# Kernel optimization log

Measured on AMD Instinct MI355X. Metric: run time of the kernel, lower is better.

## Reference

```python
import jax, jax.numpy as jnp
import numpy as np

C = 64
K = 3  # kernel_size
B, H, W = 8, 128, 128


def conv2d(x, w, b, pad, groups=1):
    y = jax.lax.conv_general_dilated(
        x, w, window_strides=(1, 1), padding=[(pad, pad), (pad, pad)],
        feature_group_count=groups, dimension_numbers=('NCHW', 'OIHW', 'NCHW'))
    return y + b[None, :, None, None]


def setup_inputs() -> dict:
    key = jax.random.key(0)
    ks = jax.random.split(key, 11)
    s3 = 1.0 / np.sqrt(C * 9)  # kaiming-ish scale for 3x3 convs
    inp = {
        'x':  jax.random.normal(ks[0], (B, C, H, W), jnp.float32),
        'w0': jax.random.normal(ks[1], (C, C, 3, 3), jnp.float32) * s3,
        'b0': jax.random.normal(ks[2], (C,), jnp.float32) * 0.01,
        'w1': jax.random.normal(ks[3], (C, 1, 3, 3), jnp.float32) * (1.0 / 3.0),  # depthwise
        'b1': jax.random.normal(ks[4], (C,), jnp.float32) * 0.01,
        'w2': jax.random.normal(ks[5], (1, 1, K), jnp.float32) * (1.0 / np.sqrt(K)),  # conv1d over channel axis
        'b2': jax.random.normal(ks[6], (1,), jnp.float32) * 0.01,
        'w3': jax.random.normal(ks[7], (C * K * K, C, 1, 1), jnp.float32) * (1.0 / np.sqrt(C)),  # 1x1 -> dynamic filters
        'b3': jax.random.normal(ks[8], (C * K * K,), jnp.float32) * 0.01,
        'wf': jax.random.normal(ks[9], (C, C, 3, 3), jnp.float32) * s3,
        'bf': jax.random.normal(ks[10], (C,), jnp.float32) * 0.01,
    }
    return inp


def reference(x, w0, b0, w1, b1, w2, b2, w3, b3, wf, bf):
    b, c, h, w = x.shape
    pre = x
    # conv0: dense 3x3
    x0 = conv2d(x, w0, b0, pad=1)
    # conv1: depthwise 3x3
    x1 = conv2d(x0, w1, b1, pad=1, groups=c)
    # ECA-style channel attention: global avg pool -> conv1d over channel dim
    m = jnp.mean(x0, axis=(2, 3))  # [b, c]
    x2 = jax.lax.conv_general_dilated(
        m[:, None, :], w2, window_strides=(1,), padding=[(K // 2, K // 2)],
        dimension_numbers=('NCH', 'OIH', 'NCH')) + b2[None, :, None]  # [b, 1, c]
    out = x1 + x2[:, 0, :, None, None]  # broadcast [b,c,1,1] over h,w
    # conv3: 1x1 producing per-pixel dynamic filters [b, c*9, h, w]
    fil = jnp.einsum('oc,bchw->bohw', w3[:, :, 0, 0], out) + b3[None, :, None, None]
    filter_x = fil.reshape(b, c, K * K, h, w)
    # unfold(x0): 3x3 patches, channel-major then row-major kernel positions
    xp = jnp.pad(x0, ((0, 0), (0, 0), (1, 1), (1, 1)))
    unfold_x = jnp.stack(
        [xp[:, :, i:i + h, j:j + w] for i in range(3) for j in range(3)], axis=2)  # [b,c,9,h,w]
    out = jnp.sum(unfold_x * filter_x, axis=2)  # per-pixel dynamic conv
    out = jnp.where(out >= 0, out, 0.2 * out)  # LeakyReLU(0.2)
    out = conv2d(out, wf, bf, pad=1) + pre
    return out
```

## Files before the change

kernel.cpp:

```cpp
#include <hip/hip_runtime.h>

#define BB 8
#define C 64
#define HH 128
#define WW 128
#define HW (HH*WW)

#define TS 72
#define NPX 324
#define FNPX 340

typedef __attribute__((ext_vector_type(8))) short short8;
typedef __attribute__((ext_vector_type(4))) short short4v;
typedef __attribute__((ext_vector_type(4))) float f32x4;

__device__ inline unsigned short f2bf(float f) {
    union { float f; unsigned u; } v; v.f = f;
    unsigned r = v.u + 0x7fff + ((v.u >> 16) & 1);
    return (unsigned short)(r >> 16);
}
__device__ inline float bf2f(unsigned short h) {
    union { unsigned u; float f; } v; v.u = ((unsigned)h) << 16;
    return v.f;
}

__global__ __launch_bounds__(256) void prep_kernel(
    const float* __restrict__ w0, const float* __restrict__ wf,
    const float* __restrict__ w3, const float* __restrict__ b3,
    unsigned short* __restrict__ wb0, unsigned short* __restrict__ wbf,
    unsigned short* __restrict__ wb3, float* __restrict__ b3r,
    float* __restrict__ m)
{
    const int t = blockIdx.x * 256 + threadIdx.x;
    for (int i = t; i < C*C*9; i += 32*256) {
        int p = i % 9; int rest = i / 9; int ci = rest % C; int oc = rest / C;
        wb0[(p*C + oc)*C + ci] = f2bf(w0[i]);
        wbf[(p*C + oc)*C + ci] = f2bf(wf[i]);
    }
    for (int i = t; i < 9*C*C; i += 32*256) {
        int j = i >> 12, oc = (i >> 6) & 63, k = i & 63;
        wb3[i] = f2bf(w3[(oc*9 + j)*C + k]);
    }
    for (int i = t; i < 9*C; i += 32*256) {
        int j = i >> 6, oc = i & 63;
        b3r[i] = b3[oc*9 + j];
    }
    for (int i = t; i < BB*C; i += 32*256) m[i] = 0.f;
}

__global__ __launch_bounds__(256) void nhwc_kernel(
    const float* __restrict__ x, unsigned short* __restrict__ xb)
{
    const int px = blockIdx.x * 256 + threadIdx.x;
    const int b = px >> 14, pin = px & 16383;
    const float* sp = x + (size_t)b*C*HW + pin;
    unsigned short* dp = xb + (size_t)px*C;
#pragma unroll
    for (int g = 0; g < 8; ++g) {
        short8 o;
#pragma unroll
        for (int k = 0; k < 8; ++k) o[k] = (short)f2bf(sp[(size_t)(g*8+k)*HW]);
        *(short8*)&dp[g*8] = o;
    }
}

__global__ __launch_bounds__(512) void conv0_kernel(
    const unsigned short* __restrict__ xb,
    const unsigned short* __restrict__ wb,
    const float* __restrict__ bias,
    unsigned short* __restrict__ x0g,
    float* __restrict__ msum)
{
    __shared__ unsigned short tile[NPX*TS];
    __shared__ float red[8][64];
    const int b  = blockIdx.z;
    const int h0 = blockIdx.y * 16;
    const int w0 = blockIdx.x * 16;
    const int t  = threadIdx.x;

    {
        const int pxi = t & 63, g = t >> 6;
        for (int px = pxi; px < NPX; px += 64) {
            int th = px / 18, tw = px - th*18;
            int gh = h0 + th - 1, gw = w0 + tw - 1;
            short8 v = {0,0,0,0,0,0,0,0};
            if ((unsigned)gh < HH && (unsigned)gw < WW)
                v = *(const short8*)&xb[((size_t)(b*HW) + gh*WW + gw)*C + g*8];
            *(short8*)&tile[px*TS + g*8] = v;
        }
    }
    __syncthreads();

    const int wid = t >> 6, ln = t & 63;
    const int l15 = ln & 15, q = ln >> 4;

    f32x4 acc[2][4];
#pragma unroll
    for (int nt = 0; nt < 2; ++nt)
#pragma unroll
        for (int mt = 0; mt < 4; ++mt) acc[nt][mt] = (f32x4){0.f,0.f,0.f,0.f};

#pragma unroll
    for (int p = 0; p < 9; ++p) {
        const int dh = p / 3, dw = p % 3;
#pragma unroll
        for (int ks = 0; ks < 2; ++ks) {
            short8 af[4];
#pragma unroll
            for (int mt = 0; mt < 4; ++mt)
                af[mt] = *(const short8*)&wb[((size_t)(p*C) + mt*16 + l15)*C + ks*32 + q*8];
            short8 bf[2];
#pragma unroll
            for (int nt = 0; nt < 2; ++nt)
                bf[nt] = *(const short8*)&tile[((wid*2+nt+dh)*18 + l15 + dw)*TS + ks*32 + q*8];
#pragma unroll
            for (int nt = 0; nt < 2; ++nt)
#pragma unroll
                for (int mt = 0; mt < 4; ++mt)
                    acc[nt][mt] = __builtin_amdgcn_mfma_f32_16x16x32_bf16(
                        af[mt], bf[nt], acc[nt][mt], 0, 0, 0);
        }
    }

#pragma unroll
    for (int nt = 0; nt < 2; ++nt) {
        const int hh = h0 + wid*2 + nt;
        const size_t base = ((size_t)(b*HW) + hh*WW + w0 + l15)*C;
#pragma unroll
        for (int mt = 0; mt < 4; ++mt) {
            const int oc0 = mt*16 + q*4;
            const float4 bv = *(const float4*)&bias[oc0];
            unsigned u0 = (unsigned)f2bf(acc[nt][mt][0] + bv.x)
                        | ((unsigned)f2bf(acc[nt][mt][1] + bv.y) << 16);
            unsigned u1 = (unsigned)f2bf(acc[nt][mt][2] + bv.z)
                        | ((unsigned)f2bf(acc[nt][mt][3] + bv.w) << 16);
            uint2 uu; uu.x = u0; uu.y = u1;
            *(uint2*)&x0g[base + oc0] = uu;
        }
    }

    f32x4 s[4];
#pragma unroll
    for (int mt = 0; mt < 4; ++mt)
#pragma unroll
        for (int reg = 0; reg < 4; ++reg)
            s[mt][reg] = acc[0][mt][reg] + acc[1][mt][reg];
#pragma unroll
    for (int mask = 1; mask < 16; mask <<= 1)
#pragma unroll
        for (int mt = 0; mt < 4; ++mt)
#pragma unroll
            for (int reg = 0; reg < 4; ++reg)
                s[mt][reg] += __shfl_xor(s[mt][reg], mask);
    if (l15 == 0) {
#pragma unroll
        for (int mt = 0; mt < 4; ++mt)
#pragma unroll
            for (int reg = 0; reg < 4; ++reg)
                red[wid][mt*16 + q*4 + reg] = s[mt][reg];
    }
    __syncthreads();
    if (t < 64) {
        float tot = bias[t] * 256.f;
#pragma unroll
        for (int w = 0; w < 8; ++w) tot += red[w][t];
        atomicAdd(&msum[b*C + t], tot);
    }
}

__global__ __launch_bounds__(512) void fused_dyn_kernel(
    const unsigned short* __restrict__ x0,
    const float* __restrict__ w1, const float* __restrict__ b1,
    const float* __restrict__ w2, const float* __restrict__ b2,
    const unsigned short* __restrict__ wb3,
    const float* __restrict__ b3r,
    const float* __restrict__ m,
    unsigned short* __restrict__ yg)
{
    __shared__ unsigned short tile[NPX*TS];
    __shared__ unsigned short alds[256*64];
    const int b  = blockIdx.z;
    const int h0 = blockIdx.y * 16;
    const int w0 = blockIdx.x * 16;
    const int t  = threadIdx.x;

    {
        const int pxi = t & 63, g = t >> 6;
        for (int px = pxi; px < NPX; px += 64) {
            int th = px / 18, tw = px - th*18;
            int gh = h0 + th - 1, gw = w0 + tw - 1;
            short8 v = {0,0,0,0,0,0,0,0};
            if ((unsigned)gh < HH && (unsigned)gw < WW)
                v = *(const short8*)&x0[((size_t)(b*HW) + gh*WW + gw)*C + g*8];
            *(short8*)&tile[px*TS + g*8] = v;
        }
    }
    __syncthreads();

    {
        const int px = t & 255, ghalf = t >> 8;
        const int r = px >> 4, cc = px & 15;
        const unsigned short* tb = tile + (r*18 + cc)*TS;
        const float w2a = w2[0], w2b = w2[1], w2c = w2[2], b2v = b2[0];
        const float inv = 1.f / (float)HW;
        const int sw = px & 7;
#pragma unroll
        for (int g = 0; g < 4; ++g) {
            const int octet = ghalf*4 + g;
            float dw8[8];
#pragma unroll
            for (int k = 0; k < 8; ++k) dw8[k] = 0.f;
#pragma unroll
            for (int j = 0; j < 9; ++j) {
                short8 v = *(const short8*)&tb[((j/3)*18 + (j%3))*TS + octet*8];
#pragma unroll
                for (int k = 0; k < 8; ++k)
                    dw8[k] = fmaf(w1[(octet*8+k)*9 + j],
                                  bf2f((unsigned short)v[k]), dw8[k]);
            }
            short8 o;
#pragma unroll
            for (int k = 0; k < 8; ++k) {
                const int c = octet*8 + k;
                const float mc = m[b*C + c] * inv;
                const float mp = (c > 0)  ? m[b*C + c - 1] * inv : 0.f;
                const float mn = (c < 63) ? m[b*C + c + 1] * inv : 0.f;
                const float att = fmaf(w2a, mp, fmaf(w2b, mc, fmaf(w2c, mn, b2v)));
                o[k] = (short)f2bf(dw8[k] + b1[c] + att);
            }
            *(short8*)&alds[px*64 + ((octet ^ sw) * 8)] = o;
        }
    }
    __syncthreads();

    const int wid = t >> 6, ln = t & 63;
    const int l15 = ln & 15, q = ln >> 4;
    const int rl0 = (wid & 3) * 4;
    const int ogh = wid >> 2;

    short8 pfrag[4][2];
#pragma unroll
    for (int nt = 0; nt < 4; ++nt) {
        const int p = (rl0 + nt)*16 + l15;
        const int psw = p & 7;
#pragma unroll
        for (int ks = 0; ks < 2; ++ks)
            pfrag[nt][ks] = *(const short8*)&alds[p*64 + (((ks*4 + q) ^ psw) * 8)];
    }

#pragma unroll
    for (int ogi = 0; ogi < 2; ++ogi) {
        const int og = ogh*2 + ogi;
        f32x4 yac[4];
#pragma unroll
        for (int nt = 0; nt < 4; ++nt) yac[nt] = (f32x4){0.f,0.f,0.f,0.f};

        for (int j = 0; j < 9; ++j) {
            const int dh = j / 3, dw = j - dh*3;
            const f32x4 seed = *(const f32x4*)&b3r[j*64 + og*16 + q*4];
            const size_t abase = ((size_t)(j*64 + og*16 + l15))*C;
            const short8 a0 = *(const short8*)&wb3[abase + q*8];
            const short8 a1 = *(const short8*)&wb3[abase + 32 + q*8];
#pragma unroll
            for (int nt = 0; nt < 4; ++nt) {
                f32x4 fil = __builtin_amdgcn_mfma_f32_16x16x32_bf16(
                    a0, pfrag[nt][0], seed, 0, 0, 0);
                fil = __builtin_amdgcn_mfma_f32_16x16x32_bf16(
                    a1, pfrag[nt][1], fil, 0, 0, 0);
                const short4v pv = *(const short4v*)
                    &tile[((rl0+nt+dh)*18 + l15 + dw)*TS + og*16 + q*4];
#pragma unroll
                for (int reg = 0; reg < 4; ++reg)
                    yac[nt][reg] = fmaf(fil[reg],
                        bf2f((unsigned short)pv[reg]), yac[nt][reg]);
            }
        }

#pragma unroll
        for (int nt = 0; nt < 4; ++nt) {
            const size_t base = ((size_t)(b*HW) + (h0+rl0+nt)*WW + w0 + l15)*C;
            f32x4 v = yac[nt];
#pragma unroll
            for (int reg = 0; reg < 4; ++reg)
                v[reg] = (v[reg] >= 0.f) ? v[reg] : 0.2f * v[reg];
            unsigned u0 = (unsigned)f2bf(v[0]) | ((unsigned)f2bf(v[1]) << 16);
            unsigned u1 = (unsigned)f2bf(v[2]) | ((unsigned)f2bf(v[3]) << 16);
            uint2 uu; uu.x = u0; uu.y = u1;
            *(uint2*)&yg[base + og*16 + q*4] = uu;
        }
    }
}

__global__ __launch_bounds__(512) void convf_kernel(
    const unsigned short* __restrict__ yg,
    const unsigned short* __restrict__ wb,
    const float* __restrict__ bias,
    const float* __restrict__ res,
    float* __restrict__ outg)
{
    __shared__ unsigned short tile[FNPX*TS];
    const int b  = blockIdx.z;
    const int h0 = blockIdx.y * 8;
    const int w0 = blockIdx.x * 32;
    const int t  = threadIdx.x;

    {
        const int pxi = t & 63, g = t >> 6;
        for (int px = pxi; px < FNPX; px += 64) {
            int th = px / 34, tw = px - th*34;
            int gh = h0 + th - 1, gw = w0 + tw - 1;
            short8 v = {0,0,0,0,0,0,0,0};
            if ((unsigned)gh < HH && (unsigned)gw < WW)
                v = *(const short8*)&yg[((size_t)(b*HW) + gh*WW + gw)*C + g*8];
            *(short8*)&tile[px*TS + g*8] = v;
        }
    }
    __syncthreads();

    const int wid = t >> 6, ln = t & 63;
    const int l15 = ln & 15, q = ln >> 4;

    f32x4 acc[2][4];
#pragma unroll
    for (int mg = 0; mg < 2; ++mg)
#pragma unroll
        for (int nt = 0; nt < 4; ++nt) acc[mg][nt] = (f32x4){0.f,0.f,0.f,0.f};

#pragma unroll
    for (int p = 0; p < 9; ++p) {
        const int dh = p / 3, dw = p % 3;
#pragma unroll
        for (int ks = 0; ks < 2; ++ks) {
            short8 bfrag[4];
#pragma unroll
            for (int nt = 0; nt < 4; ++nt)
                bfrag[nt] = *(const short8*)&wb[((size_t)(p*C) + nt*16 + l15)*C + ks*32 + q*8];
            short8 afrag[2];
#pragma unroll
            for (int mg = 0; mg < 2; ++mg)
                afrag[mg] = *(const short8*)&tile[((wid+dh)*34 + mg*16 + l15 + dw)*TS + ks*32 + q*8];
#pragma unroll
            for (int mg = 0; mg < 2; ++mg)
#pragma unroll
                for (int nt = 0; nt < 4; ++nt)
                    acc[mg][nt] = __builtin_amdgcn_mfma_f32_16x16x32_bf16(
                        afrag[mg], bfrag[nt], acc[mg][nt], 0, 0, 0);
        }
    }

#pragma unroll
    for (int mg = 0; mg < 2; ++mg) {
#pragma unroll
        for (int nt = 0; nt < 4; ++nt) {
            const int oc = nt*16 + l15;
            const float bv = bias[oc];
            const size_t base = (size_t)(b*C + oc)*HW + (h0+wid)*WW + w0 + mg*16 + q*4;
            const float4 rv = *(const float4*)&res[base];
            float4 ov;
            ov.x = acc[mg][nt][0] + bv + rv.x;
            ov.y = acc[mg][nt][1] + bv + rv.y;
            ov.z = acc[mg][nt][2] + bv + rv.z;
            ov.w = acc[mg][nt][3] + bv + rv.w;
            *(float4*)&outg[base] = ov;
        }
    }
}

extern "C" void kernel_launch(void* const* d_in, const int* in_sizes, int n_in,
                              void* d_out, int out_size, void* d_ws, size_t ws_size,
                              hipStream_t stream) {
    const float* x  = (const float*)d_in[0];
    const float* w0 = (const float*)d_in[1];
    const float* b0 = (const float*)d_in[2];
    const float* w1 = (const float*)d_in[3];
    const float* b1 = (const float*)d_in[4];
    const float* w2 = (const float*)d_in[5];
    const float* b2 = (const float*)d_in[6];
    const float* w3 = (const float*)d_in[7];
    const float* b3 = (const float*)d_in[8];
    const float* wf = (const float*)d_in[9];
    const float* bf = (const float*)d_in[10];
    float* out = (float*)d_out;

    unsigned short* x0  = (unsigned short*)d_ws;
    unsigned short* y   = x0  + (size_t)BB*HW*C;
    unsigned short* xb  = y   + (size_t)BB*HW*C;
    float*          m   = (float*)(xb + (size_t)BB*HW*C);
    unsigned short* wb0 = (unsigned short*)(m + BB*C);
    unsigned short* wbf = wb0 + 9*C*C;
    unsigned short* wb3 = wbf + 9*C*C;
    float*          b3r = (float*)(wb3 + 9*C*C);

    prep_kernel<<<32, 256, 0, stream>>>(w0, wf, w3, b3, wb0, wbf, wb3, b3r, m);
    nhwc_kernel<<<512, 256, 0, stream>>>(x, xb);
    conv0_kernel<<<dim3(8,8,8), 512, 0, stream>>>(xb, wb0, b0, x0, m);
    fused_dyn_kernel<<<dim3(8,8,8), 512, 0, stream>>>(
        x0, w1, b1, w2, b2, wb3, b3r, m, y);
    convf_kernel<<<dim3(4,16,8), 512, 0, stream>>>(y, wbf, bf, x, out);
}
```

Measured before the change: 248.2 us.

## Halve spatial tiles and block size; batch all halo loads before LDS stores

Each of the three conv kernels now uses half-height tiles with 256 threads instead of 512, doubling the grid to 1024 blocks so more blocks fit per CU and the GPU fills better. The halo tile load is rewritten so every thread issues all of its global loads into registers before any LDS store, putting more memory requests in flight. The cost is a larger fraction of redundant halo rows per output, twice as many atomics into the channel-mean sum, and changed warp-to-work mapping in the dynamic-filter stage.

```diff
diff --git a/kernel.cpp b/kernel.cpp
--- a/kernel.cpp
+++ b/kernel.cpp
@@ -7,8 +7,8 @@
 #define HW (HH*WW)
 
 #define TS 72
-#define NPX 324
-#define FNPX 340
+#define NPXC 180
+#define NPXF 204
 
 typedef __attribute__((ext_vector_type(8))) short short8;
 typedef __attribute__((ext_vector_type(4))) short short4v;
@@ -64,29 +64,39 @@
     }
 }
 
-__global__ __launch_bounds__(512) void conv0_kernel(
+__global__ __launch_bounds__(256) void conv0_kernel(
     const unsigned short* __restrict__ xb,
     const unsigned short* __restrict__ wb,
     const float* __restrict__ bias,
     unsigned short* __restrict__ x0g,
     float* __restrict__ msum)
 {
-    __shared__ unsigned short tile[NPX*TS];
-    __shared__ float red[8][64];
+    __shared__ unsigned short tile[NPXC*TS];
+    __shared__ float red[4][64];
     const int b  = blockIdx.z;
-    const int h0 = blockIdx.y * 16;
+    const int h0 = blockIdx.y * 8;
     const int w0 = blockIdx.x * 16;
     const int t  = threadIdx.x;
 
     {
-        const int pxi = t & 63, g = t >> 6;
-        for (int px = pxi; px < NPX; px += 64) {
-            int th = px / 18, tw = px - th*18;
-            int gh = h0 + th - 1, gw = w0 + tw - 1;
-            short8 v = {0,0,0,0,0,0,0,0};
-            if ((unsigned)gh < HH && (unsigned)gw < WW)
-                v = *(const short8*)&xb[((size_t)(b*HW) + gh*WW + gw)*C + g*8];
-            *(short8*)&tile[px*TS + g*8] = v;
+        short8 v[6];
+#pragma unroll
+        for (int k = 0; k < 6; ++k) {
+            const int ci = t + k*256;
+            v[k] = (short8){0,0,0,0,0,0,0,0};
+            if (ci < NPXC*8) {
+                const int px = ci >> 3, g = ci & 7;
+                const int th = px / 18, tw = px - th*18;
+                const int gh = h0 + th - 1, gw = w0 + tw - 1;
+                if ((unsigned)gh < HH && (unsigned)gw < WW)
+                    v[k] = *(const short8*)&xb[((size_t)(b*HW) + gh*WW + gw)*C + g*8];
+            }
+        }
+#pragma unroll
+        for (int k = 0; k < 6; ++k) {
+            const int ci = t + k*256;
+            if (ci < NPXC*8)
+                *(short8*)&tile[(ci >> 3)*TS + (ci & 7)*8] = v[k];
         }
     }
     __syncthreads();
@@ -161,14 +171,14 @@
     }
     __syncthreads();
     if (t < 64) {
-        float tot = bias[t] * 256.f;
-#pragma unroll
-        for (int w = 0; w < 8; ++w) tot += red[w][t];
+        float tot = bias[t] * 128.f;
+#pragma unroll
+        for (int w = 0; w < 4; ++w) tot += red[w][t];
         atomicAdd(&msum[b*C + t], tot);
     }
 }
 
-__global__ __launch_bounds__(512) void fused_dyn_kernel(
+__global__ __launch_bounds__(256) void fused_dyn_kernel(
     const unsigned short* __restrict__ x0,
     const float* __restrict__ w1, const float* __restrict__ b1,
     const float* __restrict__ w2, const float* __restrict__ b2,
@@ -177,28 +187,38 @@
     const float* __restrict__ m,
     unsigned short* __restrict__ yg)
 {
-    __shared__ unsigned short tile[NPX*TS];
-    __shared__ unsigned short alds[256*64];
+    __shared__ unsigned short tile[NPXC*TS];
+    __shared__ unsigned short alds[128*64];
     const int b  = blockIdx.z;
-    const int h0 = blockIdx.y * 16;
+    const int h0 = blockIdx.y * 8;
     const int w0 = blockIdx.x * 16;
     const int t  = threadIdx.x;
 
     {
-        const int pxi = t & 63, g = t >> 6;
-        for (int px = pxi; px < NPX; px += 64) {
-            int th = px / 18, tw = px - th*18;
-            int gh = h0 + th - 1, gw = w0 + tw - 1;
-            short8 v = {0,0,0,0,0,0,0,0};
-            if ((unsigned)gh < HH && (unsigned)gw < WW)
-                v = *(const short8*)&x0[((size_t)(b*HW) + gh*WW + gw)*C + g*8];
-            *(short8*)&tile[px*TS + g*8] = v;
+        short8 v[6];
+#pragma unroll
+        for (int k = 0; k < 6; ++k) {
+            const int ci = t + k*256;
+            v[k] = (short8){0,0,0,0,0,0,0,0};
+            if (ci < NPXC*8) {
+                const int px = ci >> 3, g = ci & 7;
+                const int th = px / 18, tw = px - th*18;
+                const int gh = h0 + th - 1, gw = w0 + tw - 1;
+                if ((unsigned)gh < HH && (unsigned)gw < WW)
+                    v[k] = *(const short8*)&x0[((size_t)(b*HW) + gh*WW + gw)*C + g*8];
+            }
+        }
+#pragma unroll
+        for (int k = 0; k < 6; ++k) {
+            const int ci = t + k*256;
+            if (ci < NPXC*8)
+                *(short8*)&tile[(ci >> 3)*TS + (ci & 7)*8] = v[k];
         }
     }
     __syncthreads();
 
     {
-        const int px = t & 255, ghalf = t >> 8;
+        const int px = t & 127, ghalf = t >> 7;
         const int r = px >> 4, cc = px & 15;
         const unsigned short* tb = tile + (r*18 + cc)*TS;
         const float w2a = w2[0], w2b = w2[1], w2c = w2[2], b2v = b2[0];
@@ -235,13 +255,11 @@
 
     const int wid = t >> 6, ln = t & 63;
     const int l15 = ln & 15, q = ln >> 4;
-    const int rl0 = (wid & 3) * 4;
-    const int ogh = wid >> 2;
-
-    short8 pfrag[4][2];
-#pragma unroll
-    for (int nt = 0; nt < 4; ++nt) {
-        const int p = (rl0 + nt)*16 + l15;
+
+    short8 pfrag[2][2];
+#pragma unroll
+    for (int nt = 0; nt < 2; ++nt) {
+        const int p = (wid*2 + nt)*16 + l15;
         const int psw = p & 7;
 #pragma unroll
         for (int ks = 0; ks < 2; ++ks)
@@ -249,11 +267,10 @@
     }
 
 #pragma unroll
-    for (int ogi = 0; ogi < 2; ++ogi) {
-        const int og = ogh*2 + ogi;
-        f32x4 yac[4];
-#pragma unroll
-        for (int nt = 0; nt < 4; ++nt) yac[nt] = (f32x4){0.f,0.f,0.f,0.f};
+    for (int og = 0; og < 4; ++og) {
+        f32x4 yac[2];
+#pragma unroll
+        for (int nt = 0; nt < 2; ++nt) yac[nt] = (f32x4){0.f,0.f,0.f,0.f};
 
         for (int j = 0; j < 9; ++j) {
             const int dh = j / 3, dw = j - dh*3;
@@ -262,13 +279,14 @@
             const short8 a0 = *(const short8*)&wb3[abase + q*8];
             const short8 a1 = *(const short8*)&wb3[abase + 32 + q*8];
 #pragma unroll
-            for (int nt = 0; nt < 4; ++nt) {
+            for (int nt = 0; nt < 2; ++nt) {
+                const int rr = wid*2 + nt;
                 f32x4 fil = __builtin_amdgcn_mfma_f32_16x16x32_bf16(
                     a0, pfrag[nt][0], seed, 0, 0, 0);
                 fil = __builtin_amdgcn_mfma_f32_16x16x32_bf16(
                     a1, pfrag[nt][1], fil, 0, 0, 0);
                 const short4v pv = *(const short4v*)
-                    &tile[((rl0+nt+dh)*18 + l15 + dw)*TS + og*16 + q*4];
+                    &tile[((rr+dh)*18 + l15 + dw)*TS + og*16 + q*4];
 #pragma unroll
                 for (int reg = 0; reg < 4; ++reg)
                     yac[nt][reg] = fmaf(fil[reg],
@@ -277,8 +295,9 @@
         }
 
 #pragma unroll
-        for (int nt = 0; nt < 4; ++nt) {
-            const size_t base = ((size_t)(b*HW) + (h0+rl0+nt)*WW + w0 + l15)*C;
+        for (int nt = 0; nt < 2; ++nt) {
+            const int rr = wid*2 + nt;
+            const size_t base = ((size_t)(b*HW) + (h0+rr)*WW + w0 + l15)*C;
             f32x4 v = yac[nt];
 #pragma unroll
             for (int reg = 0; reg < 4; ++reg)
@@ -291,28 +310,38 @@
     }
 }
 
-__global__ __launch_bounds__(512) void convf_kernel(
+__global__ __launch_bounds__(256) void convf_kernel(
     const unsigned short* __restrict__ yg,
     const unsigned short* __restrict__ wb,
     const float* __restrict__ bias,
     const float* __restrict__ res,
     float* __restrict__ outg)
 {
-    __shared__ unsigned short tile[FNPX*TS];
+    __shared__ unsigned short tile[NPXF*TS];
     const int b  = blockIdx.z;
-    const int h0 = blockIdx.y * 8;
+    const int h0 = blockIdx.y * 4;
     const int w0 = blockIdx.x * 32;
     const int t  = threadIdx.x;
 
     {
-        const int pxi = t & 63, g = t >> 6;
-        for (int px = pxi; px < FNPX; px += 64) {
-            int th = px / 34, tw = px - th*34;
-            int gh = h0 + th - 1, gw = w0 + tw - 1;
-            short8 v = {0,0,0,0,0,0,0,0};
-            if ((unsigned)gh < HH && (unsigned)gw < WW)
-                v = *(const short8*)&yg[((size_t)(b*HW) + gh*WW + gw)*C + g*8];
-            *(short8*)&tile[px*TS + g*8] = v;
+        short8 v[7];
+#pragma unroll
+        for (int k = 0; k < 7; ++k) {
+            const int ci = t + k*256;
+            v[k] = (short8){0,0,0,0,0,0,0,0};
+            if (ci < NPXF*8) {
+                const int px = ci >> 3, g = ci & 7;
+                const int th = px / 34, tw = px - th*34;
+                const int gh = h0 + th - 1, gw = w0 + tw - 1;
+                if ((unsigned)gh < HH && (unsigned)gw < WW)
+                    v[k] = *(const short8*)&yg[((size_t)(b*HW) + gh*WW + gw)*C + g*8];
+            }
+        }
+#pragma unroll
+        for (int k = 0; k < 7; ++k) {
+            const int ci = t + k*256;
+            if (ci < NPXF*8)
+                *(short8*)&tile[(ci >> 3)*TS + (ci & 7)*8] = v[k];
         }
     }
     __syncthreads();
@@ -393,8 +422,8 @@
 
     prep_kernel<<<32, 256, 0, stream>>>(w0, wf, w3, b3, wb0, wbf, wb3, b3r, m);
     nhwc_kernel<<<512, 256, 0, stream>>>(x, xb);
-    conv0_kernel<<<dim3(8,8,8), 512, 0, stream>>>(xb, wb0, b0, x0, m);
-    fused_dyn_kernel<<<dim3(8,8,8), 512, 0, stream>>>(
+    conv0_kernel<<<dim3(8,16,8), 256, 0, stream>>>(xb, wb0, b0, x0, m);
+    fused_dyn_kernel<<<dim3(8,16,8), 256, 0, stream>>>(
         x0, w1, b1, w2, b2, wb3, b3r, m, y);
-    convf_kernel<<<dim3(4,16,8), 512, 0, stream>>>(y, wbf, bf, x, out);
-}
+    convf_kernel<<<dim3(4,32,8), 256, 0, stream>>>(y, wbf, bf, x, out);
+}
```

Measured after the change: 260.7 us. 1.05x slower.
